# Kernel optimization log

Measured on AMD Instinct MI355X. Metric: run time of the kernel, lower is better.

The kernel has to match this reference:

```python
import jax, jax.numpy as jnp
import numpy as np

B, S, HID = 2, 2048, 2048
NH, NG = 32, 8
HD = HID // NH  # 64
KV = HD * NG    # 512


def setup_inputs() -> dict:
    key = jax.random.key(0)
    ks = jax.random.split(key, 9)
    w = lambda k, shp: jax.random.normal(k, shp, dtype=jnp.float32) * 0.02
    return {
        "hidden_state": jax.random.normal(ks[0], (B, S, HID), dtype=jnp.float32),
        "Wq": w(ks[1], (HID, HID)), "bq": jnp.zeros((HID,), jnp.float32),
        "Wk": w(ks[2], (HID, KV)),  "bk": jnp.zeros((KV,), jnp.float32),
        "Wv": w(ks[3], (HID, KV)),  "bv": jnp.zeros((KV,), jnp.float32),
        "Wo": w(ks[4], (HID, HID)), "bo": jnp.zeros((HID,), jnp.float32),
    }


def reference(hidden_state, Wq, bq, Wk, bk, Wv, bv, Wo, bo):
    bs, seq, _ = hidden_state.shape
    rep = NH // NG  # heads per KV group

    q = hidden_state @ Wq + bq                      # [B,S,HID]
    k = hidden_state @ Wk + bk                      # [B,S,KV]
    v = hidden_state @ Wv + bv

    q = q.reshape(bs, seq, NH, HD).transpose(0, 2, 1, 3)   # [B,NH,S,D]
    k = k.reshape(bs, seq, NG, HD).transpose(0, 2, 1, 3)   # [B,NG,S,D]
    v = v.reshape(bs, seq, NG, HD).transpose(0, 2, 1, 3)
    # grouped-KV expansion: each group repeated consecutively rep times
    k = jnp.repeat(k, rep, axis=1)                          # [B,NH,S,D]
    v = jnp.repeat(v, rep, axis=1)

    scores = jnp.einsum("bhqd,bhkd->bhqk", q, k) / jnp.sqrt(jnp.float32(HD))
    probs = jax.nn.softmax(scores, axis=-1)
    out = jnp.einsum("bhqk,bhkd->bhqd", probs, v)           # [B,NH,S,D]
    out = out.transpose(0, 2, 1, 3).reshape(bs, seq, HID)
    return out @ Wo + bo
```

## Files before the change

### kernel.cpp

```cpp
#include <hip/hip_runtime.h>
#include <hip/hip_bf16.h>
#include <math.h>

typedef __bf16 bf16x8 __attribute__((ext_vector_type(8)));
typedef float f32x4 __attribute__((ext_vector_type(4)));
typedef __hip_bfloat16 bf16_t;

#define MFMA_BF16(a, b, c) __builtin_amdgcn_mfma_f32_16x16x32_bf16((a), (b), (c), 0, 0, 0)

__device__ __forceinline__ void async_copy16(const bf16_t* g, bf16_t* lds_base) {
  __builtin_amdgcn_global_load_lds(
      (const __attribute__((address_space(1))) unsigned int*)g,
      (__attribute__((address_space(3))) unsigned int*)lds_base,
      16, 0, 0);
}

__device__ __forceinline__ unsigned fbits(float x) { return __builtin_bit_cast(unsigned, x); }

__global__ __launch_bounds__(256) void prep(
    const float* __restrict__ hidden, const float* __restrict__ Wq, const float* __restrict__ Wk,
    const float* __restrict__ Wv, const float* __restrict__ Wo,
    const float* __restrict__ bq, const float* __restrict__ bk, const float* __restrict__ bv,
    bf16_t* __restrict__ hiddenB, bf16_t* __restrict__ WqkvT, bf16_t* __restrict__ WoT,
    float* __restrict__ bqkv, float c1) {
  __shared__ float tile[64][65];
  int bid = blockIdx.x;
  const int t = threadIdx.x;
  if (bid < 8192) {
    const int i = bid * 256 + t;
    float4 v = ((const float4*)hidden)[i];
    union { bf16_t h[4]; ushort4 u; } cv;
    cv.h[0] = __float2bfloat16(v.x);
    cv.h[1] = __float2bfloat16(v.y);
    cv.h[2] = __float2bfloat16(v.z);
    cv.h[3] = __float2bfloat16(v.w);
    ((ushort4*)hiddenB)[i] = cv.u;
    return;
  }
  bid -= 8192;
  if (bid >= 2560) {
    const int i = (bid - 2560) * 256 + t;
    float v;
    if (i < 2048) v = bq[i] * c1;
    else if (i < 2560) v = bk[i - 2048];
    else v = bv[i - 2560];
    bqkv[i] = v;
    return;
  }
  const float* src;
  bf16_t* dst;
  int Cc, bx, by;
  float scale = 1.0f;
  if (bid < 1024) { src = Wq; dst = WqkvT; Cc = 2048; bx = bid & 31; by = bid >> 5; scale = c1; }
  else if (bid < 1280) { bid -= 1024; src = Wk; dst = WqkvT + (size_t)2048 * 2048; Cc = 512; bx = bid & 7; by = bid >> 3; }
  else if (bid < 1536) { bid -= 1280; src = Wv; dst = WqkvT + (size_t)2560 * 2048; Cc = 512; bx = bid & 7; by = bid >> 3; }
  else { bid -= 1536; src = Wo; dst = WoT; Cc = 2048; bx = bid & 31; by = bid >> 5; }
  const int tx = t & 63, ty = t >> 6;
  const int c0 = bx * 64, r0 = by * 64;
#pragma unroll
  for (int i = ty; i < 64; i += 4)
    tile[i][tx] = src[(size_t)(r0 + i) * Cc + c0 + tx];
  __syncthreads();
#pragma unroll
  for (int i = ty; i < 64; i += 4)
    dst[(size_t)(c0 + i) * 2048 + r0 + tx] = __float2bfloat16(tile[tx][i] * scale);
}

template <typename TOUT>
__global__ __launch_bounds__(256, 3) void gemm_bt(
    const bf16_t* __restrict__ A, const bf16_t* __restrict__ Bt,
    const float* __restrict__ bias, TOUT* __restrict__ C, bf16_t* __restrict__ vTp,
    int M, int N, int K) {
  __shared__ alignas(16) bf16_t As[128 * 64];
  __shared__ alignas(16) bf16_t Bs[128 * 64];

  const int tid = threadIdx.x;
  const int w = tid >> 6, lane = tid & 63;
  const int quad = lane >> 4, l16 = lane & 15;
  const int wm = w >> 1, wn = w & 1;
  const int m0 = blockIdx.y * 128, n0 = blockIdx.x * 128;

  f32x4 acc[4][4] = {};

  const int rr = lane >> 3;
  const int scol = ((lane & 7) ^ rr) * 8;
  const int sx = l16 & 7;

  for (int k0 = 0; k0 < K; k0 += 64) {
    __syncthreads();
#pragma unroll
    for (int c = 0; c < 4; ++c) {
      const int r = w * 32 + c * 8 + rr;
      async_copy16(A + (size_t)(m0 + r) * K + k0 + scol, &As[(w * 32 + c * 8) * 64]);
      async_copy16(Bt + (size_t)(n0 + r) * K + k0 + scol, &Bs[(w * 32 + c * 8) * 64]);
    }
    __syncthreads();

#pragma unroll
    for (int kh = 0; kh < 2; ++kh) {
      bf16x8 af[4], bf[4];
#pragma unroll
      for (int i = 0; i < 4; ++i) {
        af[i] = *(const bf16x8*)&As[(wm * 64 + i * 16 + l16) * 64 + (((kh * 4 + quad) ^ sx) * 8)];
        bf[i] = *(const bf16x8*)&Bs[(wn * 64 + i * 16 + l16) * 64 + (((kh * 4 + quad) ^ sx) * 8)];
      }
#pragma unroll
      for (int i = 0; i < 4; ++i)
#pragma unroll
        for (int j = 0; j < 4; ++j)
          acc[i][j] = MFMA_BF16(af[i], bf[j], acc[i][j]);
    }
  }

  if (vTp != nullptr && n0 >= 2560) {
#pragma unroll
    for (int i = 0; i < 4; ++i) {
      const int row = m0 + wm * 64 + i * 16 + quad * 4;
      const int bb = row >> 11, s = row & 2047;
#pragma unroll
      for (int j = 0; j < 4; ++j) {
        const int col = n0 + wn * 64 + j * 16 + l16;
        const float bv = bias[col];
        union { bf16_t h[4]; ushort4 u; } cv;
#pragma unroll
        for (int r = 0; r < 4; ++r) cv.h[r] = __float2bfloat16(acc[i][j][r] + bv);
        *(ushort4*)&vTp[((size_t)bb * 512 + (col - 2560)) * 2048 + s] = cv.u;
      }
    }
    return;
  }

#pragma unroll
  for (int i = 0; i < 4; ++i) {
    const int row = m0 + wm * 64 + i * 16 + quad * 4;
#pragma unroll
    for (int j = 0; j < 4; ++j) {
      const int col = n0 + wn * 64 + j * 16 + l16;
      const float bv = bias[col];
#pragma unroll
      for (int r = 0; r < 4; ++r) {
        const float val = acc[i][j][r] + bv;
        if constexpr (__is_same(TOUT, float)) {
          C[(size_t)(row + r) * N + col] = val;
        } else {
          C[(size_t)(row + r) * N + col] = __float2bfloat16(val);
        }
      }
    }
  }
}

__global__ __launch_bounds__(256, 4) void gqa_attn(
    const bf16_t* __restrict__ QKV, const bf16_t* __restrict__ VT, bf16_t* __restrict__ O) {
  constexpr int S = 2048, HID = 2048, QKVS = 3072, HD = 64;
  const int tid = threadIdx.x;
  const int w = tid >> 6, lane = tid & 63;
  const int quad = lane >> 4, l16 = lane & 15;
  const int hp = blockIdx.y, b = blockIdx.z;
  const int h = hp * 2 + (w & 1);
  const int g = hp >> 1;
  const int q0 = blockIdx.x * 64 + (w >> 1) * 32;

  __shared__ alignas(16) bf16_t Ks[64 * 64];
  __shared__ alignas(16) bf16_t VTs[64 * 64];
  __shared__ alignas(16) bf16_t Ps[128 * 64];

  bf16x8 qf[2][2];
#pragma unroll
  for (int mt = 0; mt < 2; ++mt)
#pragma unroll
    for (int ks = 0; ks < 2; ++ks)
      qf[mt][ks] = *(const bf16x8*)&QKV[(size_t)(b * S + q0 + mt * 16 + l16) * QKVS +
                                        h * HD + ks * 32 + quad * 8];

  const int rr = lane >> 3, c7 = lane & 7;
  const int sx = l16 & 7;

  const bf16_t* Kbase = QKV + (size_t)b * S * QKVS + 2048 + g * HD;
  const bf16_t* Vbase = VT + (size_t)(b * 512 + g * HD) * S;

  const int srow = w * 16 + rr;
  const bf16_t* kp0 = Kbase + (size_t)srow * QKVS + c7 * 8;
  const bf16_t* kp1 = kp0 + (size_t)8 * QKVS;
  const bf16_t* vp0 = Vbase + (size_t)srow * S + c7 * 8;
  const bf16_t* vp1 = vp0 + (size_t)8 * S;
  bf16_t* KsW0 = &Ks[(srow)*64 + (c7 ^ rr) * 8];
  bf16_t* KsW1 = KsW0 + 8 * 64;
  bf16_t* VsW0 = &VTs[(srow)*64 + (c7 ^ rr) * 8];
  bf16_t* VsW1 = VsW0 + 8 * 64;

  f32x4 oacc[2][4] = {};
  f32x4 lacc[2] = {};
  bf16x8 ones;
#pragma unroll
  for (int j = 0; j < 8; ++j) ones[j] = (__bf16)1.0f;

  uint4 kr0 = *(const uint4*)kp0;
  uint4 kr1 = *(const uint4*)kp1;
  uint4 vr0 = *(const uint4*)vp0;
  uint4 vr1 = *(const uint4*)vp1;

  for (int s0 = 0; s0 < S; s0 += 64) {
    __syncthreads();
    *(uint4*)KsW0 = kr0;
    *(uint4*)KsW1 = kr1;
    *(uint4*)VsW0 = vr0;
    *(uint4*)VsW1 = vr1;
    const int sn = (s0 + 64) & (S - 1);
    kr0 = *(const uint4*)(kp0 + (size_t)sn * QKVS);
    kr1 = *(const uint4*)(kp1 + (size_t)sn * QKVS);
    vr0 = *(const uint4*)(vp0 + sn);
    vr1 = *(const uint4*)(vp1 + sn);
    __syncthreads();

    __builtin_amdgcn_s_setprio(1);
#pragma unroll
    for (int nt = 0; nt < 4; ++nt) {
      bf16x8 kf0 = *(const bf16x8*)&Ks[(nt * 16 + l16) * 64 + ((quad ^ sx) * 8)];
      bf16x8 kf1 = *(const bf16x8*)&Ks[(nt * 16 + l16) * 64 + (((4 + quad) ^ sx) * 8)];
#pragma unroll
      for (int mt = 0; mt < 2; ++mt) {
        f32x4 s = {};
        s = MFMA_BF16(kf0, qf[mt][0], s);
        s = MFMA_BF16(kf1, qf[mt][1], s);
        const float p0 = __builtin_amdgcn_exp2f(s[0]);
        const float p1 = __builtin_amdgcn_exp2f(s[1]);
        const float p2 = __builtin_amdgcn_exp2f(s[2]);
        const float p3 = __builtin_amdgcn_exp2f(s[3]);
        uint2 pk;
        pk.x = __builtin_amdgcn_perm(fbits(p1), fbits(p0), 0x07060302);
        pk.y = __builtin_amdgcn_perm(fbits(p3), fbits(p2), 0x07060302);
        *(uint2*)&Ps[(w * 32 + mt * 16 + l16) * 64 +
                     (((nt * 2 + (quad >> 1)) ^ sx) * 8) + (quad & 1) * 4] = pk;
      }
    }

#pragma unroll
    for (int kc = 0; kc < 2; ++kc) {
      bf16x8 pf[2];
#pragma unroll
      for (int mt = 0; mt < 2; ++mt) {
        pf[mt] = *(const bf16x8*)&Ps[(w * 32 + mt * 16 + l16) * 64 + (((kc * 4 + quad) ^ sx) * 8)];
        lacc[mt] = MFMA_BF16(pf[mt], ones, lacc[mt]);
      }
#pragma unroll
      for (int dt = 0; dt < 4; ++dt) {
        bf16x8 vf = *(const bf16x8*)&VTs[(dt * 16 + l16) * 64 + (((kc * 4 + quad) ^ sx) * 8)];
#pragma unroll
        for (int mt = 0; mt < 2; ++mt)
          oacc[mt][dt] = MFMA_BF16(pf[mt], vf, oacc[mt][dt]);
      }
    }
    __builtin_amdgcn_s_setprio(0);
  }

#pragma unroll
  for (int mt = 0; mt < 2; ++mt) {
    float linv[4];
#pragma unroll
    for (int r = 0; r < 4; ++r) linv[r] = 1.0f / lacc[mt][r];
#pragma unroll
    for (int dt = 0; dt < 4; ++dt)
#pragma unroll
      for (int r = 0; r < 4; ++r)
        O[(size_t)(b * S + q0 + mt * 16 + quad * 4 + r) * HID + h * HD + dt * 16 + l16] =
            __float2bfloat16(oacc[mt][dt][r] * linv[r]);
  }
}

extern "C" void kernel_launch(void* const* d_in, const int* in_sizes, int n_in,
                              void* d_out, int out_size, void* d_ws, size_t ws_size,
                              hipStream_t stream) {
  const float* hidden = (const float*)d_in[0];
  const float* Wq = (const float*)d_in[1];
  const float* bq = (const float*)d_in[2];
  const float* Wk = (const float*)d_in[3];
  const float* bk = (const float*)d_in[4];
  const float* Wv = (const float*)d_in[5];
  const float* bv = (const float*)d_in[6];
  const float* Wo = (const float*)d_in[7];
  const float* bo = (const float*)d_in[8];
  float* out = (float*)d_out;

  constexpr int B = 2, S = 2048, HID = 2048, KV = 512, QKVN = 3072;
  constexpr int M = B * S;
  const float c1 = 0.125f * 1.44269504089f;

  char* ws = (char*)d_ws;
  bf16_t* hiddenB = (bf16_t*)ws; ws += (size_t)M * HID * 2;
  bf16_t* WqkvT = (bf16_t*)ws;   ws += (size_t)QKVN * HID * 2;
  bf16_t* WoT = (bf16_t*)ws;     ws += (size_t)HID * HID * 2;
  bf16_t* qkv = (bf16_t*)ws;     ws += (size_t)M * QKVN * 2;
  bf16_t* vT = (bf16_t*)ws;      ws += (size_t)M * KV * 2;
  bf16_t* attn = (bf16_t*)ws;    ws += (size_t)M * HID * 2;
  float* bqkv = (float*)ws;      ws += QKVN * 4;

  prep<<<8192 + 2560 + 12, 256, 0, stream>>>(hidden, Wq, Wk, Wv, Wo, bq, bk, bv,
                                             hiddenB, WqkvT, WoT, bqkv, c1);

  gemm_bt<bf16_t><<<dim3(QKVN / 128, M / 128), 256, 0, stream>>>(
      hiddenB, WqkvT, bqkv, qkv, vT, M, QKVN, HID);

  gqa_attn<<<dim3(S / 64, 16, B), 256, 0, stream>>>(qkv, vT, attn);

  gemm_bt<float><<<dim3(HID / 128, M / 128), 256, 0, stream>>>(
      attn, WoT, bo, out, (bf16_t*)nullptr, M, HID, HID);
}
```

Before: 302.5 us.

## Add 256x256-tile 8-wave pipelined GEMM for the QKV projection

Replaces the 128x128 QKV projection GEMM with a new kernel that uses 256x256 tiles, 512 threads and double-buffered async global-to-LDS loads with XOR-swizzled shared memory. Loads of the next k-tile are interleaved with the MFMA phases, and there are explicit barriers and priority raises around the math. The larger tile raises arithmetic intensity and the pipeline is meant to overlap memory latency with compute. In exchange the grid shrinks to 12x16=192 blocks, which may underfill the CUs, and register and LDS pressure goes up.

```diff
diff --git a/kernel.cpp b/kernel.cpp
--- a/kernel.cpp
+++ b/kernel.cpp
@@ -150,6 +150,143 @@
   }
 }
 
+__global__ __launch_bounds__(512, 2) void gemm256(
+    const bf16_t* __restrict__ A, const bf16_t* __restrict__ Bt,
+    const float* __restrict__ bias, bf16_t* __restrict__ C, bf16_t* __restrict__ vTp) {
+  constexpr int N = 3072, K = 2048;
+  __shared__ alignas(16) bf16_t As[2 * 256 * 64];
+  __shared__ alignas(16) bf16_t Bs[2 * 256 * 64];
+
+  const int tid = threadIdx.x;
+  const int w = tid >> 6, lane = tid & 63;
+  const int quad = lane >> 4, l16 = lane & 15;
+  const int wm = w >> 2, wn = w & 3;
+  const int m0 = blockIdx.y * 256, n0 = blockIdx.x * 256;
+
+  const int rr = lane >> 3, c7 = lane & 7;
+  const int scol = (c7 ^ rr) * 8;
+  const int sx = l16 & 7;
+
+  auto stA = [&](int t, int h) {
+    const int kb = (t & 31) * 64;
+    const int rbase = h * 128 + w * 8;
+    bf16_t* d0 = &As[(t & 1) * (256 * 64) + rbase * 64];
+    const bf16_t* s0 = A + (size_t)(m0 + rbase + rr) * K + kb + scol;
+    async_copy16(s0, d0);
+    async_copy16(s0 + (size_t)64 * K, d0 + 64 * 64);
+  };
+  auto stB = [&](int t, int h) {
+    const int kb = (t & 31) * 64;
+    const int rbase = h * 128 + w * 8;
+    bf16_t* d0 = &Bs[(t & 1) * (256 * 64) + rbase * 64];
+    const bf16_t* s0 = Bt + (size_t)(n0 + rbase + rr) * K + kb + scol;
+    async_copy16(s0, d0);
+    async_copy16(s0 + (size_t)64 * K, d0 + 64 * 64);
+  };
+
+  f32x4 acc[4][2][4] = {};
+
+  stB(0, 0); stB(0, 1); stA(0, 0); stA(0, 1);
+  stB(1, 0); stB(1, 1);
+  asm volatile("s_waitcnt vmcnt(4)" ::: "memory");
+  __builtin_amdgcn_sched_barrier(0);
+  __builtin_amdgcn_s_barrier();
+  __builtin_amdgcn_sched_barrier(0);
+
+  for (int it = 0; it < 16; ++it) {
+    const int kt = it * 2;
+#pragma unroll
+    for (int kg = 0; kg < 2; ++kg) {
+      const int ta = (kt + kg + 1) & 31;
+      const int tb = (kt + kg + 2) & 31;
+      const bf16_t* Asb = &As[kg * (256 * 64)];
+      const bf16_t* Bsb = &Bs[kg * (256 * 64)];
+      bf16x8 b[4][2];
+#pragma unroll
+      for (int p = 0; p < 4; ++p) {
+        if (p == 0) {
+#pragma unroll
+          for (int ni = 0; ni < 4; ++ni)
+#pragma unroll
+            for (int kk = 0; kk < 2; ++kk)
+              b[ni][kk] = *(const bf16x8*)&Bsb[(wn * 64 + ni * 16 + l16) * 64 +
+                                               (((kk * 4 + quad) ^ sx) * 8)];
+        }
+        bf16x8 a[2][2];
+#pragma unroll
+        for (int mi = 0; mi < 2; ++mi)
+#pragma unroll
+          for (int kk = 0; kk < 2; ++kk)
+            a[mi][kk] = *(const bf16x8*)&Asb[(wm * 128 + p * 32 + mi * 16 + l16) * 64 +
+                                             (((kk * 4 + quad) ^ sx) * 8)];
+        if (p == 0) stA(ta, 0);
+        else if (p == 1) stA(ta, 1);
+        else if (p == 2) stB(tb, 0);
+        else stB(tb, 1);
+        __builtin_amdgcn_sched_barrier(0);
+        __builtin_amdgcn_s_barrier();
+        __builtin_amdgcn_sched_barrier(0);
+        asm volatile("s_waitcnt lgkmcnt(0)" ::: "memory");
+        __builtin_amdgcn_sched_barrier(0);
+        __builtin_amdgcn_s_setprio(1);
+#pragma unroll
+        for (int kk = 0; kk < 2; ++kk)
+#pragma unroll
+          for (int mi = 0; mi < 2; ++mi)
+#pragma unroll
+            for (int ni = 0; ni < 4; ++ni)
+              acc[p][mi][ni] = MFMA_BF16(a[mi][kk], b[ni][kk], acc[p][mi][ni]);
+        __builtin_amdgcn_s_setprio(0);
+        __builtin_amdgcn_sched_barrier(0);
+        if (p == 3) {
+          asm volatile("s_waitcnt vmcnt(4)" ::: "memory");
+          __builtin_amdgcn_sched_barrier(0);
+        }
+        __builtin_amdgcn_s_barrier();
+        __builtin_amdgcn_sched_barrier(0);
+      }
+    }
+  }
+
+  asm volatile("s_waitcnt vmcnt(0)" ::: "memory");
+  __builtin_amdgcn_sched_barrier(0);
+
+  if (n0 >= 2560) {
+#pragma unroll
+    for (int p = 0; p < 4; ++p)
+#pragma unroll
+      for (int mi = 0; mi < 2; ++mi) {
+        const int row4 = m0 + wm * 128 + p * 32 + mi * 16 + quad * 4;
+        const int bb = row4 >> 11, s = row4 & 2047;
+#pragma unroll
+        for (int ni = 0; ni < 4; ++ni) {
+          const int col = n0 + wn * 64 + ni * 16 + l16;
+          const float bv = bias[col];
+          union { bf16_t h[4]; ushort4 u; } cv;
+#pragma unroll
+          for (int r = 0; r < 4; ++r) cv.h[r] = __float2bfloat16(acc[p][mi][ni][r] + bv);
+          *(ushort4*)&vTp[((size_t)bb * 512 + (col - 2560)) * 2048 + s] = cv.u;
+        }
+      }
+    return;
+  }
+
+#pragma unroll
+  for (int p = 0; p < 4; ++p)
+#pragma unroll
+    for (int mi = 0; mi < 2; ++mi) {
+      const int row4 = m0 + wm * 128 + p * 32 + mi * 16 + quad * 4;
+#pragma unroll
+      for (int ni = 0; ni < 4; ++ni) {
+        const int col = n0 + wn * 64 + ni * 16 + l16;
+        const float bv = bias[col];
+#pragma unroll
+        for (int r = 0; r < 4; ++r)
+          C[(size_t)(row4 + r) * N + col] = __float2bfloat16(acc[p][mi][ni][r] + bv);
+      }
+    }
+}
+
 __global__ __launch_bounds__(256, 4) void gqa_attn(
     const bf16_t* __restrict__ QKV, const bf16_t* __restrict__ VT, bf16_t* __restrict__ O) {
   constexpr int S = 2048, HID = 2048, QKVS = 3072, HD = 64;
@@ -298,8 +435,7 @@
   prep<<<8192 + 2560 + 12, 256, 0, stream>>>(hidden, Wq, Wk, Wv, Wo, bq, bk, bv,
                                              hiddenB, WqkvT, WoT, bqkv, c1);
 
-  gemm_bt<bf16_t><<<dim3(QKVN / 128, M / 128), 256, 0, stream>>>(
-      hiddenB, WqkvT, bqkv, qkv, vT, M, QKVN, HID);
+  gemm256<<<dim3(QKVN / 256, M / 256), 512, 0, stream>>>(hiddenB, WqkvT, bqkv, qkv, vT);
 
   gqa_attn<<<dim3(S / 64, 16, B), 256, 0, stream>>>(qkv, vT, attn);
 
```

Result: no change. 301.7 us (-0.3%).
